# Kernel optimization log

Measured on AMD Instinct MI355X. Metric: run time of the kernel, lower is better.

Reference implementation:

```python
import jax, jax.numpy as jnp
import numpy as np
import math

CLASSES = 1024
IN_F = 32
OUT_F = 32
N = 262144


def setup_inputs() -> dict:
    key = jax.random.key(0)
    k1, k2, k3, k4 = jax.random.split(key, 4)
    k = math.sqrt(1.0 / float(IN_F))
    inp = jax.random.normal(k1, (N, IN_F), dtype=jnp.float32)
    inds = jax.random.randint(k2, (N,), 0, CLASSES, dtype=jnp.int32)
    w = jax.random.uniform(k3, (CLASSES, IN_F, OUT_F), dtype=jnp.float32, minval=-k, maxval=k)
    b = jax.random.uniform(k4, (CLASSES, 1, OUT_F), dtype=jnp.float32, minval=-k, maxval=k)
    return {"input": inp, "inds": inds, "w": w, "b": b}


def reference(input, inds, w, b):
    # per-row expert matmul: out[n] = input[n] @ w[inds[n]] + b[inds[n]]
    w_g = w[inds]            # [n, in, out] gathered expert weights
    b_g = b[inds, 0]         # [n, out]
    return jnp.einsum('ni,nio->no', input, w_g) + b_g
```

## Files before the change

### kernel.cpp

```cpp
#include <hip/hip_runtime.h>


#define N_ROWS      262144
#define N_CLASSES   1024
#define IN_F        32
#define OUT_F       32
#define HB          64
#define ROWS_PER_HB (N_ROWS / HB)

__global__ __launch_bounds__(256) void k_hist(const int* __restrict__ inds,
                                              int* __restrict__ bcT) {
    __shared__ int h[N_CLASSES];
    const int tid = threadIdx.x;
    for (int c = tid; c < N_CLASSES; c += 256) h[c] = 0;
    __syncthreads();
    const int base = blockIdx.x * ROWS_PER_HB;
    for (int k = 0; k < ROWS_PER_HB; k += 256)
        atomicAdd(&h[inds[base + k + tid]], 1);
    __syncthreads();
    for (int c = tid; c < N_CLASSES; c += 256)
        bcT[c * HB + blockIdx.x] = h[c];
}

__global__ __launch_bounds__(1024) void k_scan(const int* __restrict__ bcT,
                                               int* __restrict__ cls_off) {
    __shared__ int s[N_CLASSES];
    const int c = threadIdx.x;
    const int4* p = (const int4*)(bcT + c * HB);
    int total = 0;
#pragma unroll
    for (int j = 0; j < HB / 4; ++j) {
        const int4 t = p[j];
        total += t.x + t.y + t.z + t.w;
    }
    s[c] = total;
    __syncthreads();
    for (int off = 1; off < N_CLASSES; off <<= 1) {
        int v = (c >= off) ? s[c - off] : 0;
        __syncthreads();
        s[c] += v;
        __syncthreads();
    }
    cls_off[c] = s[c] - total;
    if (c == N_CLASSES - 1) cls_off[N_CLASSES] = s[c];
}

__global__ __launch_bounds__(256) void k_offsets(int* __restrict__ bcT,
                                                 const int* __restrict__ cls_off) {
    const int c = blockIdx.x * 256 + threadIdx.x;
    int run = cls_off[c];
    int4* p = (int4*)(bcT + c * HB);
#pragma unroll
    for (int j = 0; j < HB / 4; ++j) {
        const int4 t = p[j];
        int4 o;
        o.x = run; run += t.x;
        o.y = run; run += t.y;
        o.z = run; run += t.z;
        o.w = run; run += t.w;
        p[j] = o;
    }
}

__global__ __launch_bounds__(256) void k_scatter(const int* __restrict__ inds,
                                                 const int* __restrict__ bcT,
                                                 int* __restrict__ rowids) {
    __shared__ int cur[N_CLASSES];
    const int tid = threadIdx.x;
    for (int c = tid; c < N_CLASSES; c += 256)
        cur[c] = bcT[c * HB + blockIdx.x];
    __syncthreads();
    const int base = blockIdx.x * ROWS_PER_HB;
    for (int k = 0; k < ROWS_PER_HB; k += 256) {
        const int row = base + k + tid;
        const int c = inds[row];
        const int pos = atomicAdd(&cur[c], 1);
        rowids[pos] = row;
    }
}

__global__ __launch_bounds__(512, 4) void k_condmul(const float* __restrict__ input,
                                                    const float* __restrict__ w,
                                                    const float* __restrict__ bias,
                                                    const int* __restrict__ rowids,
                                                    const int* __restrict__ cls_off,
                                                    float* __restrict__ out) {
    const int cls = blockIdx.x;
    const int tid = threadIdx.x;
    const int oq = tid & 7;
    const int kh = (tid >> 3) & 1;
    const int rg = tid >> 4;

    const int start = cls_off[cls];
    const int count = cls_off[cls + 1] - start;
    if (count <= 0) return;

    const float4* w4 = (const float4*)(w + (size_t)cls * (IN_F * OUT_F)) + (size_t)kh * 16 * (OUT_F / 4) + oq;
    float4 wk[16];
#pragma unroll
    for (int j = 0; j < 16; ++j) wk[j] = w4[(size_t)j * (OUT_F / 4)];

    const float4 bv = ((const float4*)(bias + (size_t)cls * OUT_F))[oq];

    const int iters = (count + 31) >> 5;
    for (int it = 0; it < iters; ++it) {
        const int ri = it * 32 + rg;
        const bool valid = ri < count;
        const int idx = valid ? ri : (count - 1);
        const int row = rowids[start + idx];

        const float4* xin = (const float4*)(input + (size_t)row * IN_F + kh * 16);
        float4 x[4];
#pragma unroll
        for (int j = 0; j < 4; ++j) x[j] = xin[j];

        float4 acc = {0.f, 0.f, 0.f, 0.f};
#pragma unroll
        for (int j = 0; j < 4; ++j) {
            const float a0 = x[j].x, a1 = x[j].y, a2 = x[j].z, a3 = x[j].w;
            const float4 w0 = wk[4 * j + 0];
            const float4 w1 = wk[4 * j + 1];
            const float4 w2 = wk[4 * j + 2];
            const float4 w3 = wk[4 * j + 3];
            acc.x += a0 * w0.x; acc.y += a0 * w0.y; acc.z += a0 * w0.z; acc.w += a0 * w0.w;
            acc.x += a1 * w1.x; acc.y += a1 * w1.y; acc.z += a1 * w1.z; acc.w += a1 * w1.w;
            acc.x += a2 * w2.x; acc.y += a2 * w2.y; acc.z += a2 * w2.z; acc.w += a2 * w2.w;
            acc.x += a3 * w3.x; acc.y += a3 * w3.y; acc.z += a3 * w3.z; acc.w += a3 * w3.w;
        }
        acc.x += __shfl_xor(acc.x, 8);
        acc.y += __shfl_xor(acc.y, 8);
        acc.z += __shfl_xor(acc.z, 8);
        acc.w += __shfl_xor(acc.w, 8);

        if (valid && kh == 0) {
            float4 o;
            o.x = acc.x + bv.x;
            o.y = acc.y + bv.y;
            o.z = acc.z + bv.z;
            o.w = acc.w + bv.w;
            ((float4*)(out + (size_t)row * OUT_F))[oq] = o;
        }
    }
}

__global__ __launch_bounds__(256) void k_naive(const float* __restrict__ input,
                                               const int* __restrict__ inds,
                                               const float* __restrict__ w,
                                               const float* __restrict__ bias,
                                               float* __restrict__ out) {
    const int tid = threadIdx.x;
    const int oq = tid & 7;
    const int rg = tid >> 3;
    const int row = blockIdx.x * 32 + rg;
    if (row >= N_ROWS) return;
    const int c = inds[row];
    const float4* xin = (const float4*)(input + (size_t)row * IN_F);
    const float4* wr = (const float4*)(w + (size_t)c * IN_F * OUT_F);
    float4 acc = ((const float4*)(bias + (size_t)c * OUT_F))[oq];
#pragma unroll
    for (int j = 0; j < 8; ++j) {
        const float4 xv = xin[j];
        const float a0 = xv.x, a1 = xv.y, a2 = xv.z, a3 = xv.w;
        const float4 w0 = wr[(j * 4 + 0) * (OUT_F / 4) + oq];
        const float4 w1 = wr[(j * 4 + 1) * (OUT_F / 4) + oq];
        const float4 w2 = wr[(j * 4 + 2) * (OUT_F / 4) + oq];
        const float4 w3 = wr[(j * 4 + 3) * (OUT_F / 4) + oq];
        acc.x += a0 * w0.x; acc.y += a0 * w0.y; acc.z += a0 * w0.z; acc.w += a0 * w0.w;
        acc.x += a1 * w1.x; acc.y += a1 * w1.y; acc.z += a1 * w1.z; acc.w += a1 * w1.w;
        acc.x += a2 * w2.x; acc.y += a2 * w2.y; acc.z += a2 * w2.z; acc.w += a2 * w2.w;
        acc.x += a3 * w3.x; acc.y += a3 * w3.y; acc.z += a3 * w3.z; acc.w += a3 * w3.w;
    }
    ((float4*)(out + (size_t)row * OUT_F))[oq] = acc;
}

extern "C" void kernel_launch(void* const* d_in, const int* in_sizes, int n_in,
                              void* d_out, int out_size, void* d_ws, size_t ws_size,
                              hipStream_t stream) {
    const float* input = (const float*)d_in[0];
    const int*   inds  = (const int*)d_in[1];
    const float* w     = (const float*)d_in[2];
    const float* bias  = (const float*)d_in[3];
    float* out = (float*)d_out;

    int* ws = (int*)d_ws;
    int* bcT     = ws;
    int* cls_off = ws + N_CLASSES * HB;
    int* rowids  = cls_off + N_CLASSES + 1 + 3;
    const size_t need = (size_t)(N_CLASSES * HB + N_CLASSES + 4 + N_ROWS) * sizeof(int);

    if (ws_size >= need) {
        k_hist<<<HB, 256, 0, stream>>>(inds, bcT);
        k_scan<<<1, 1024, 0, stream>>>(bcT, cls_off);
        k_offsets<<<N_CLASSES / 256, 256, 0, stream>>>(bcT, cls_off);
        k_scatter<<<HB, 256, 0, stream>>>(inds, bcT, rowids);
        k_condmul<<<N_CLASSES, 512, 0, stream>>>(input, w, bias, rowids, cls_off, out);
    } else {
        k_naive<<<N_ROWS / 32, 256, 0, stream>>>(input, inds, w, bias, out);
    }
}
```

Before: 138.6 us.

## Fuse offset computation into scan and shrink condmul blocks to 256 threads

The per-block offset computation is folded into the scan kernel, dropping one kernel launch and a reread of the count matrix. The scan kernel now writes the per-block running offsets back itself, which puts a serial loop on the single-block scan. The grouped matmul kernel uses 256-thread blocks processing 16 rows per iteration, and its weights are pinned in VGPRs with empty asm barriers. The inner loop is manually unrolled. Smaller blocks reduce idle lanes for small classes but double the iteration count per class.

```diff
diff --git a/kernel.cpp b/kernel.cpp
--- a/kernel.cpp
+++ b/kernel.cpp
@@ -22,11 +22,11 @@
         bcT[c * HB + blockIdx.x] = h[c];
 }
 
-__global__ __launch_bounds__(1024) void k_scan(const int* __restrict__ bcT,
+__global__ __launch_bounds__(1024) void k_scan(int* __restrict__ bcT,
                                                int* __restrict__ cls_off) {
     __shared__ int s[N_CLASSES];
     const int c = threadIdx.x;
-    const int4* p = (const int4*)(bcT + c * HB);
+    int4* p = (int4*)(bcT + c * HB);
     int total = 0;
 #pragma unroll
     for (int j = 0; j < HB / 4; ++j) {
@@ -41,15 +41,9 @@
         s[c] += v;
         __syncthreads();
     }
-    cls_off[c] = s[c] - total;
+    int run = s[c] - total;
+    cls_off[c] = run;
     if (c == N_CLASSES - 1) cls_off[N_CLASSES] = s[c];
-}
-
-__global__ __launch_bounds__(256) void k_offsets(int* __restrict__ bcT,
-                                                 const int* __restrict__ cls_off) {
-    const int c = blockIdx.x * 256 + threadIdx.x;
-    int run = cls_off[c];
-    int4* p = (int4*)(bcT + c * HB);
 #pragma unroll
     for (int j = 0; j < HB / 4; ++j) {
         const int4 t = p[j];
@@ -79,7 +73,7 @@
     }
 }
 
-__global__ __launch_bounds__(512, 4) void k_condmul(const float* __restrict__ input,
+__global__ __launch_bounds__(256, 4) void k_condmul(const float* __restrict__ input,
                                                     const float* __restrict__ w,
                                                     const float* __restrict__ bias,
                                                     const int* __restrict__ rowids,
@@ -95,38 +89,60 @@
     const int count = cls_off[cls + 1] - start;
     if (count <= 0) return;
 
-    const float4* w4 = (const float4*)(w + (size_t)cls * (IN_F * OUT_F)) + (size_t)kh * 16 * (OUT_F / 4) + oq;
+    const float4* w4 = (const float4*)(w + (size_t)cls * (IN_F * OUT_F))
+                       + (size_t)(kh * 16) * (OUT_F / 4) + oq;
     float4 wk[16];
 #pragma unroll
     for (int j = 0; j < 16; ++j) wk[j] = w4[(size_t)j * (OUT_F / 4)];
+#pragma unroll
+    for (int j = 0; j < 16; ++j)
+        asm volatile("" : "+v"(wk[j].x), "+v"(wk[j].y), "+v"(wk[j].z), "+v"(wk[j].w));
 
     const float4 bv = ((const float4*)(bias + (size_t)cls * OUT_F))[oq];
 
-    const int iters = (count + 31) >> 5;
+    const int iters = (count + 15) >> 4;
     for (int it = 0; it < iters; ++it) {
-        const int ri = it * 32 + rg;
+        const int ri = it * 16 + rg;
         const bool valid = ri < count;
         const int idx = valid ? ri : (count - 1);
         const int row = rowids[start + idx];
 
         const float4* xin = (const float4*)(input + (size_t)row * IN_F + kh * 16);
-        float4 x[4];
-#pragma unroll
-        for (int j = 0; j < 4; ++j) x[j] = xin[j];
+        const float4 x0 = xin[0];
+        const float4 x1 = xin[1];
+        const float4 x2 = xin[2];
+        const float4 x3 = xin[3];
 
         float4 acc = {0.f, 0.f, 0.f, 0.f};
-#pragma unroll
-        for (int j = 0; j < 4; ++j) {
-            const float a0 = x[j].x, a1 = x[j].y, a2 = x[j].z, a3 = x[j].w;
-            const float4 w0 = wk[4 * j + 0];
-            const float4 w1 = wk[4 * j + 1];
-            const float4 w2 = wk[4 * j + 2];
-            const float4 w3 = wk[4 * j + 3];
-            acc.x += a0 * w0.x; acc.y += a0 * w0.y; acc.z += a0 * w0.z; acc.w += a0 * w0.w;
-            acc.x += a1 * w1.x; acc.y += a1 * w1.y; acc.z += a1 * w1.z; acc.w += a1 * w1.w;
-            acc.x += a2 * w2.x; acc.y += a2 * w2.y; acc.z += a2 * w2.z; acc.w += a2 * w2.w;
-            acc.x += a3 * w3.x; acc.y += a3 * w3.y; acc.z += a3 * w3.z; acc.w += a3 * w3.w;
-        }
+        {
+            const float a0 = x0.x, a1 = x0.y, a2 = x0.z, a3 = x0.w;
+            acc.x += a0 * wk[0].x;  acc.y += a0 * wk[0].y;  acc.z += a0 * wk[0].z;  acc.w += a0 * wk[0].w;
+            acc.x += a1 * wk[1].x;  acc.y += a1 * wk[1].y;  acc.z += a1 * wk[1].z;  acc.w += a1 * wk[1].w;
+            acc.x += a2 * wk[2].x;  acc.y += a2 * wk[2].y;  acc.z += a2 * wk[2].z;  acc.w += a2 * wk[2].w;
+            acc.x += a3 * wk[3].x;  acc.y += a3 * wk[3].y;  acc.z += a3 * wk[3].z;  acc.w += a3 * wk[3].w;
+        }
+        {
+            const float a0 = x1.x, a1 = x1.y, a2 = x1.z, a3 = x1.w;
+            acc.x += a0 * wk[4].x;  acc.y += a0 * wk[4].y;  acc.z += a0 * wk[4].z;  acc.w += a0 * wk[4].w;
+            acc.x += a1 * wk[5].x;  acc.y += a1 * wk[5].y;  acc.z += a1 * wk[5].z;  acc.w += a1 * wk[5].w;
+            acc.x += a2 * wk[6].x;  acc.y += a2 * wk[6].y;  acc.z += a2 * wk[6].z;  acc.w += a2 * wk[6].w;
+            acc.x += a3 * wk[7].x;  acc.y += a3 * wk[7].y;  acc.z += a3 * wk[7].z;  acc.w += a3 * wk[7].w;
+        }
+        {
+            const float a0 = x2.x, a1 = x2.y, a2 = x2.z, a3 = x2.w;
+            acc.x += a0 * wk[8].x;  acc.y += a0 * wk[8].y;  acc.z += a0 * wk[8].z;  acc.w += a0 * wk[8].w;
+            acc.x += a1 * wk[9].x;  acc.y += a1 * wk[9].y;  acc.z += a1 * wk[9].z;  acc.w += a1 * wk[9].w;
+            acc.x += a2 * wk[10].x; acc.y += a2 * wk[10].y; acc.z += a2 * wk[10].z; acc.w += a2 * wk[10].w;
+            acc.x += a3 * wk[11].x; acc.y += a3 * wk[11].y; acc.z += a3 * wk[11].z; acc.w += a3 * wk[11].w;
+        }
+        {
+            const float a0 = x3.x, a1 = x3.y, a2 = x3.z, a3 = x3.w;
+            acc.x += a0 * wk[12].x; acc.y += a0 * wk[12].y; acc.z += a0 * wk[12].z; acc.w += a0 * wk[12].w;
+            acc.x += a1 * wk[13].x; acc.y += a1 * wk[13].y; acc.z += a1 * wk[13].z; acc.w += a1 * wk[13].w;
+            acc.x += a2 * wk[14].x; acc.y += a2 * wk[14].y; acc.z += a2 * wk[14].z; acc.w += a2 * wk[14].w;
+            acc.x += a3 * wk[15].x; acc.y += a3 * wk[15].y; acc.z += a3 * wk[15].z; acc.w += a3 * wk[15].w;
+        }
+
         acc.x += __shfl_xor(acc.x, 8);
         acc.y += __shfl_xor(acc.y, 8);
         acc.z += __shfl_xor(acc.z, 8);
@@ -191,9 +207,8 @@
     if (ws_size >= need) {
         k_hist<<<HB, 256, 0, stream>>>(inds, bcT);
         k_scan<<<1, 1024, 0, stream>>>(bcT, cls_off);
-        k_offsets<<<N_CLASSES / 256, 256, 0, stream>>>(bcT, cls_off);
         k_scatter<<<HB, 256, 0, stream>>>(inds, bcT, rowids);
-        k_condmul<<<N_CLASSES, 512, 0, stream>>>(input, w, bias, rowids, cls_off, out);
+        k_condmul<<<N_CLASSES, 256, 0, stream>>>(input, w, bias, rowids, cls_off, out);
     } else {
         k_naive<<<N_ROWS / 32, 256, 0, stream>>>(input, inds, w, bias, out);
     }
```

Measured after the change: 149.5 us. 1.08x slower.
